# Performance work log

Measured on AMD Instinct MI355X. Metric: run time of the kernel, lower is better.

## Reference

```python
import jax, jax.numpy as jnp
import numpy as np

B, E, CIN, O = 2, 50000, 8, 128


def _mesh_conv(x, gemm, w, b):
    # MeshCNN MeshConv: x (B,C,E), gemm (B,E,4) neighbor indices, w (O,C,5), b (O,)
    # gather 4 GeMM neighbors per edge, build 5 symmetric features, 1x5 conv
    neigh = jax.vmap(lambda xb, gb: xb[:, gb])(x, gemm)  # (B,C,E,4)
    f1, f2, f3, f4 = neigh[..., 0], neigh[..., 1], neigh[..., 2], neigh[..., 3]
    G = jnp.stack([x, f1 + f3, f2 + f4, jnp.abs(f1 - f3), jnp.abs(f2 - f4)], axis=-1)  # (B,C,E,5)
    return jnp.einsum('bces,ocs->boe', G, w) + b[None, :, None]


def _inorm(x, eps=1e-5):
    # InstanceNorm (no affine, biased variance) over the edge dim, per (batch, channel)
    m = jnp.mean(x, axis=-1, keepdims=True)
    v = jnp.var(x, axis=-1, keepdims=True)
    return (x - m) * jax.lax.rsqrt(v + eps)


def _conv1(x, w, b):
    # 1x1 Conv1d: x (B,C,E), w (O,C)
    return jnp.einsum('bce,oc->boe', x, w) + b[None, :, None]


def setup_inputs() -> dict:
    key = jax.random.key(0)
    ks = jax.random.split(key, 16)

    def W(k, shape, fan):
        return jax.random.normal(k, shape, jnp.float32) * np.float32(1.0 / np.sqrt(fan))

    d = {}
    d['fe'] = jax.random.normal(ks[0], (B, CIN, E), jnp.float32)
    d['gemm'] = jax.random.randint(ks[1], (B, E, 4), 0, E)
    # first-stage MeshConvs: geometry branch (5 ch) and position branch (3 ch)
    d['w_e1'] = W(ks[2], (O, 5, 5), 25);       d['b_e1'] = jnp.zeros((O,), jnp.float32)
    d['w_p1'] = W(ks[3], (O, 3, 5), 15);       d['b_p1'] = jnp.zeros((O,), jnp.float32)
    # residual-block MeshConvs (blocks=1)
    d['w_e2'] = W(ks[4], (O, O, 5), O * 5);    d['b_e2'] = jnp.zeros((O,), jnp.float32)
    d['w_p2'] = W(ks[5], (O, O, 5), O * 5);    d['b_p2'] = jnp.zeros((O,), jnp.float32)
    # Attn(in_dim=O)
    d['wa'] = W(ks[6], (O // 4, O), O);        d['ba'] = jnp.zeros((O // 4,), jnp.float32)
    d['wb'] = W(ks[7], (O // 4, O), O);        d['bb'] = jnp.zeros((O // 4,), jnp.float32)
    d['wal'] = W(ks[8], (O // 2, O // 2), O // 2);  d['bal'] = jnp.zeros((O // 2,), jnp.float32)
    d['wbl'] = W(ks[9], (O // 2, O // 2), O // 2);  d['bbl'] = jnp.zeros((O // 2,), jnp.float32)
    d['wat'] = W(ks[10], (O // 2, O // 2, 5), O // 2 * 5); d['bat'] = jnp.zeros((O // 2,), jnp.float32)
    d['wbt'] = W(ks[11], (O // 2, O // 2, 5), O // 2 * 5); d['bbt'] = jnp.zeros((O // 2,), jnp.float32)
    d['waf'] = W(ks[12], (O, O), O);           d['baf'] = jnp.zeros((O,), jnp.float32)
    d['wbf'] = W(ks[13], (O, O), O);           d['bbf'] = jnp.zeros((O,), jnp.float32)
    return d


def reference(fe, gemm, w_e1, b_e1, w_p1, b_p1, w_e2, b_e2, w_p2, b_p2,
              wa, ba, wb, bb, wal, bal, wbl, bbl, wat, bat, wbt, bbt,
              waf, baf, wbf, bbf):
    # DownConv (8-channel input path): split into edge (5) and point (3) branches
    fe_e, fe_p = fe[:, :5, :], fe[:, 5:, :]
    x1_e = jax.nn.relu(_inorm(_mesh_conv(fe_e, gemm, w_e1, b_e1)))
    x2_e = jax.nn.relu(_inorm(_mesh_conv(x1_e, gemm, w_e2, b_e2)) + x1_e)
    x1_p = jax.nn.relu(_inorm(_mesh_conv(fe_p, gemm, w_p1, b_p1)))
    x2_p = jax.nn.relu(_inorm(_mesh_conv(x1_p, gemm, w_p2, b_p2)) + x1_p)
    # Attn fusion
    x_all = jnp.concatenate([_conv1(x2_e, wa, ba), _conv1(x2_p, wb, bb)], axis=1)  # (B, O/2, E)
    x_a_two = jnp.concatenate([_conv1(x_all, wal, bal), _mesh_conv(x_all, gemm, wat, bat)], axis=1)
    x_b_two = jnp.concatenate([_conv1(x_all, wbl, bbl), _mesh_conv(x_all, gemm, wbt, bbt)], axis=1)
    wA = jax.nn.sigmoid(_inorm(_conv1(x_a_two, waf, baf)))  # (B,O,E)
    wB = jax.nn.sigmoid(_inorm(_conv1(x_b_two, wbf, bbf)))
    weights = jax.nn.softmax(jnp.stack([wA, wB], axis=1), axis=1)  # (B,2,O,E)
    agg = x2_e * weights[:, 0] + x2_p * weights[:, 1]
    # x2_ep = cat(x2_e, x2_p); also emit the attention-fused combine (before_pool)
    return jnp.concatenate([x2_e, x2_p, agg], axis=1)  # (B, 3*O, E)
```

## Files before the change

kernel.cpp:

```cpp
#include <hip/hip_runtime.h>
#include <cstdio>
#include <math.h>


#define E_TOT 50000
#define B_TOT 2
#define TILE_E 64
#define NBLK ((E_TOT + TILE_E - 1) / TILE_E)

typedef _Float16 half_t;
typedef __attribute__((ext_vector_type(4))) _Float16 h4;
typedef __attribute__((ext_vector_type(8))) _Float16 h8;
typedef __attribute__((ext_vector_type(4))) float f32x4;

__device__ __forceinline__ float sigmoidf_(float x) {
    return 1.0f / (1.0f + __expf(-x));
}
__device__ __forceinline__ h8 habs8(h8 x) {
    union { h8 h; unsigned int u[4]; } v;
    v.h = x;
#pragma unroll
    for (int i = 0; i < 4; ++i) v.u[i] &= 0x7FFF7FFFu;
    return v.h;
}

#define OFF_W1E   0
#define OFF_W1P   8192
#define OFF_WTE2  16384
#define OFF_WTP2  98304
#define OFF_WHA   180224
#define OFF_WHB   221184
#define OFF_WTA   262144
#define OFF_WTB   266240
#define OFF_WTAF  270336
#define OFF_WTBF  286720
#define WARENA_N  303104

__global__ __launch_bounds__(256)
void wprep_k(half_t* __restrict__ wa_,
             const float* __restrict__ w_e1, const float* __restrict__ w_p1,
             const float* __restrict__ w_e2, const float* __restrict__ w_p2,
             const float* __restrict__ wat,  const float* __restrict__ wbt,
             const float* __restrict__ wa,   const float* __restrict__ wb,
             const float* __restrict__ wal,  const float* __restrict__ wbl,
             const float* __restrict__ waf,  const float* __restrict__ wbf)
{
    int idx = blockIdx.x * 256 + threadIdx.x;
    switch (blockIdx.y) {
    case 0: if (idx < 8192) { int o = idx >> 6, k = idx & 63, s = k >> 3, cc = k & 7;
            float v = (s < 5 && cc < 5) ? w_e1[o * 25 + cc * 5 + s] : 0.f;
            wa_[OFF_W1E + idx] = (half_t)v; } break;
    case 1: if (idx < 8192) { int o = idx >> 6, k = idx & 63, s = k >> 3, cc = k & 7;
            float v = (s < 5 && cc >= 5) ? w_p1[o * 15 + (cc - 5) * 5 + s] : 0.f;
            wa_[OFF_W1P + idx] = (half_t)v; } break;
    case 2: if (idx < 81920) { int o = idx / 640, r = idx % 640, s = r >> 7, c = r & 127;
            wa_[OFF_WTE2 + idx] = (half_t)w_e2[(o * 128 + c) * 5 + s]; } break;
    case 3: if (idx < 81920) { int o = idx / 640, r = idx % 640, s = r >> 7, c = r & 127;
            wa_[OFF_WTP2 + idx] = (half_t)w_p2[(o * 128 + c) * 5 + s]; } break;
    case 4: if (idx < 40960) { int o = idx / 320, r = idx % 320, s = r >> 6, c = r & 63;
            float v = (o < 64) ? (s == 0 ? wal[o * 64 + c] : 0.f)
                               : wat[((o - 64) * 64 + c) * 5 + s];
            wa_[OFF_WHA + idx] = (half_t)v; } break;
    case 5: if (idx < 40960) { int o = idx / 320, r = idx % 320, s = r >> 6, c = r & 63;
            float v = (o < 64) ? (s == 0 ? wbl[o * 64 + c] : 0.f)
                               : wbt[((o - 64) * 64 + c) * 5 + s];
            wa_[OFF_WHB + idx] = (half_t)v; } break;
    case 6: if (idx < 4096)  wa_[OFF_WTA  + idx] = (half_t)wa[idx];  break;
    case 7: if (idx < 4096)  wa_[OFF_WTB  + idx] = (half_t)wb[idx];  break;
    case 8: if (idx < 16384) wa_[OFF_WTAF + idx] = (half_t)waf[idx]; break;
    case 9: if (idx < 16384) wa_[OFF_WTBF + idx] = (half_t)wbf[idx]; break;
    }
}

__global__ __launch_bounds__(256)
void transpose_in_k(const float* __restrict__ fe, float* __restrict__ fet)
{
    int b = blockIdx.z;
    int e = blockIdx.x * 256 + threadIdx.x;
    if (e >= E_TOT) return;
    float v[8];
#pragma unroll
    for (int c = 0; c < 8; ++c)
        v[c] = fe[((long)b * 8 + c) * E_TOT + e];
    float4* dst = (float4*)&fet[((long)b * E_TOT + e) * 8];
    dst[0] = make_float4(v[0], v[1], v[2], v[3]);
    dst[1] = make_float4(v[4], v[5], v[6], v[7]);
}

__global__ __launch_bounds__(512)
void mesh1_both_k(const float* __restrict__ fet, const int* __restrict__ gemm,
                  const half_t* __restrict__ war,
                  const float* __restrict__ be1, const float* __restrict__ bp1,
                  half_t* __restrict__ tmpe, half_t* __restrict__ tmpp,
                  float* __restrict__ parte, float* __restrict__ partp)
{
    __shared__ h8 Gl[64 * 8];
    __shared__ int nidx[64][4];

    const int tid  = threadIdx.x;
    const int b    = blockIdx.y;
    const int e0   = blockIdx.x * TILE_E;
    const int lane = tid & 63;
    const int wv   = tid >> 6;
    const int l15  = lane & 15;
    const int kg   = lane >> 4;
    const int br   = wv >> 2;
    const int o0   = (wv & 3) * 32;

    const float* xb = fet + (long)b * E_TOT * 8;

    if (tid < 256) {
        int e = tid >> 2, s = tid & 3;
        int eg = e0 + e;
        nidx[e][s] = (eg < E_TOT) ? gemm[((long)b * E_TOT + eg) * 4 + s] : 0;
    }
    __syncthreads();

    {
        int e = tid >> 3, g = tid & 7;
        int eg = e0 + e;
        int se = (eg < E_TOT) ? eg : 0;
        h8 r;
        if (g == 0) {
            const float* p = xb + (long)se * 8;
            float4 v0 = *(const float4*)p, v1 = *(const float4*)(p + 4);
            r[0] = (half_t)v0.x; r[1] = (half_t)v0.y; r[2] = (half_t)v0.z; r[3] = (half_t)v0.w;
            r[4] = (half_t)v1.x; r[5] = (half_t)v1.y; r[6] = (half_t)v1.z; r[7] = (half_t)v1.w;
        } else if (g <= 4) {
            int ia = (g == 1 || g == 3) ? 0 : 1;
            const float* pa = xb + (long)nidx[e][ia] * 8;
            const float* pb = xb + (long)nidx[e][ia + 2] * 8;
            float4 a0 = *(const float4*)pa, a1 = *(const float4*)(pa + 4);
            float4 b0 = *(const float4*)pb, b1 = *(const float4*)(pb + 4);
            float aa[8] = {a0.x, a0.y, a0.z, a0.w, a1.x, a1.y, a1.z, a1.w};
            float bb[8] = {b0.x, b0.y, b0.z, b0.w, b1.x, b1.y, b1.z, b1.w};
            if (g <= 2) {
#pragma unroll
                for (int j = 0; j < 8; ++j) r[j] = (half_t)(aa[j] + bb[j]);
            } else {
#pragma unroll
                for (int j = 0; j < 8; ++j) r[j] = (half_t)fabsf(aa[j] - bb[j]);
            }
        } else {
#pragma unroll
            for (int j = 0; j < 8; ++j) r[j] = (half_t)0.f;
        }
        Gl[(e * 8 + g) ^ (e & 7)] = r;
    }
    __syncthreads();

    f32x4 acc[4][2];
#pragma unroll
    for (int mt = 0; mt < 4; ++mt)
#pragma unroll
        for (int nt = 0; nt < 2; ++nt)
#pragma unroll
            for (int j = 0; j < 4; ++j) acc[mt][nt][j] = 0.f;

    const half_t* wt = war + (br ? OFF_W1P : OFF_W1E);
#pragma unroll
    for (int ks = 0; ks < 2; ++ks) {
        h8 bw[2];
#pragma unroll
        for (int nt = 0; nt < 2; ++nt)
            bw[nt] = *(const h8*)(wt + (long)(o0 + nt * 16 + l15) * 64 + ks * 32 + kg * 8);
#pragma unroll
        for (int mt = 0; mt < 4; ++mt) {
            int row = mt * 16 + l15;
            h8 a = Gl[row * 8 + ((ks * 4 + kg) ^ (row & 7))];
#pragma unroll
            for (int nt = 0; nt < 2; ++nt)
                acc[mt][nt] = __builtin_amdgcn_mfma_f32_16x16x32_f16(a, bw[nt], acc[mt][nt], 0, 0, 0);
        }
    }

    const float* bias = br ? bp1 : be1;
    half_t* yb = (br ? tmpp : tmpe) + (long)b * E_TOT * 128;
    float* part = br ? partp : parte;
    float bv[2], s1[2], s2[2];
#pragma unroll
    for (int nt = 0; nt < 2; ++nt) {
        bv[nt] = bias[o0 + nt * 16 + l15];
        s1[nt] = 0.f; s2[nt] = 0.f;
    }
#pragma unroll
    for (int mt = 0; mt < 4; ++mt) {
        int ebase = e0 + mt * 16 + (kg << 2);
#pragma unroll
        for (int j = 0; j < 4; ++j) {
            if (ebase + j < E_TOT) {
#pragma unroll
                for (int nt = 0; nt < 2; ++nt) {
                    float v = acc[mt][nt][j] + bv[nt];
                    yb[(long)(ebase + j) * 128 + o0 + nt * 16 + l15] = (half_t)v;
                    s1[nt] += v; s2[nt] += v * v;
                }
            }
        }
    }
#pragma unroll
    for (int nt = 0; nt < 2; ++nt) {
        s1[nt] += __shfl_xor(s1[nt], 16); s1[nt] += __shfl_xor(s1[nt], 32);
        s2[nt] += __shfl_xor(s2[nt], 16); s2[nt] += __shfl_xor(s2[nt], 32);
    }
    if (lane < 16) {
        long pb = ((long)b * NBLK + blockIdx.x) * 128;
#pragma unroll
        for (int nt = 0; nt < 2; ++nt) {
            part[(pb + o0 + nt * 16 + lane) * 2 + 0] = s1[nt];
            part[(pb + o0 + nt * 16 + lane) * 2 + 1] = s2[nt];
        }
    }
}

__global__ __launch_bounds__(512)
void mesh2p_k(const half_t* __restrict__ x1e, const half_t* __restrict__ x1p,
              const int* __restrict__ gemm, const half_t* __restrict__ war,
              const float* __restrict__ be, const float* __restrict__ bp,
              half_t* __restrict__ tmpe, half_t* __restrict__ tmpp,
              float* __restrict__ parte, float* __restrict__ partp)
{
    __shared__ h8 A[1024];
    __shared__ h8 Bs[1024];
    __shared__ int nidx[64][4];

    const int tid  = threadIdx.x;
    const int br   = blockIdx.y;
    const int b    = blockIdx.z;
    const int e0   = blockIdx.x * TILE_E;
    const int lane = tid & 63;
    const int wv   = tid >> 6;
    const int l15  = lane & 15;
    const int kg   = lane >> 4;
    const int o0   = wv * 16;

    const half_t* xb = (br ? x1p : x1e) + (long)b * E_TOT * 128;
    const half_t* wt = war + (br ? OFF_WTP2 : OFF_WTE2);

    if (tid < 256) {
        int e = tid >> 2, s = tid & 3;
        int eg = e0 + e;
        nidx[e][s] = (eg < E_TOT) ? gemm[((long)b * E_TOT + eg) * 4 + s] : 0;
    }
    __syncthreads();

    int te[2], tc[2], ts[2];
#pragma unroll
    for (int t = 0; t < 2; ++t) {
        int q = t * 512 + tid;
        te[t] = q >> 4; tc[t] = q & 15;
        ts[t] = (te[t] * 16 + tc[t]) ^ (te[t] & 7);
    }

#pragma unroll
    for (int t = 0; t < 2; ++t) {
        int eg = e0 + te[t];
        int se = (eg < E_TOT) ? eg : 0;
        A[ts[t]] = *(const h8*)(xb + (long)se * 128 + tc[t] * 8);
    }
    h8 rA[2], rB[2];
#pragma unroll
    for (int t = 0; t < 2; ++t) {
        rA[t] = *(const h8*)(xb + (long)nidx[te[t]][0] * 128 + tc[t] * 8);
        rB[t] = *(const h8*)(xb + (long)nidx[te[t]][2] * 128 + tc[t] * 8);
    }
    __syncthreads();

    f32x4 acc[4];
#pragma unroll
    for (int mt = 0; mt < 4; ++mt)
#pragma unroll
        for (int j = 0; j < 4; ++j) acc[mt][j] = 0.f;

    auto chunk = [&](const h8* buf, int s) {
#pragma unroll
        for (int ks = 0; ks < 4; ++ks) {
            h8 bw = *(const h8*)(wt + ((long)(o0 + l15) * 5 + s) * 128 + ks * 32 + kg * 8);
#pragma unroll
            for (int mt = 0; mt < 4; ++mt) {
                int row = mt * 16 + l15;
                h8 a = buf[row * 16 + ((ks * 4 + kg) ^ (row & 7))];
                acc[mt] = __builtin_amdgcn_mfma_f32_16x16x32_f16(a, bw, acc[mt], 0, 0, 0);
            }
        }
    };

    chunk(A, 0);
    __syncthreads();

#pragma unroll
    for (int t = 0; t < 2; ++t) {
        Bs[ts[t]] = rA[t] + rB[t];
        A[ts[t]]  = habs8(rA[t] - rB[t]);
    }
#pragma unroll
    for (int t = 0; t < 2; ++t) {
        rA[t] = *(const h8*)(xb + (long)nidx[te[t]][1] * 128 + tc[t] * 8);
        rB[t] = *(const h8*)(xb + (long)nidx[te[t]][3] * 128 + tc[t] * 8);
    }
    __syncthreads();

    chunk(Bs, 1);
    chunk(A, 3);
    __syncthreads();

#pragma unroll
    for (int t = 0; t < 2; ++t) {
        Bs[ts[t]] = rA[t] + rB[t];
        A[ts[t]]  = habs8(rA[t] - rB[t]);
    }
    __syncthreads();

    chunk(Bs, 2);
    chunk(A, 4);

    const float* bias = br ? bp : be;
    half_t* yb = (br ? tmpp : tmpe) + (long)b * E_TOT * 128;
    float* part = br ? partp : parte;
    float bv = bias[o0 + l15];
    float s1 = 0.f, s2 = 0.f;
#pragma unroll
    for (int mt = 0; mt < 4; ++mt) {
        int ebase = e0 + mt * 16 + (kg << 2);
#pragma unroll
        for (int j = 0; j < 4; ++j) {
            if (ebase + j < E_TOT) {
                float v = acc[mt][j] + bv;
                yb[(long)(ebase + j) * 128 + o0 + l15] = (half_t)v;
                s1 += v; s2 += v * v;
            }
        }
    }
    s1 += __shfl_xor(s1, 16); s1 += __shfl_xor(s1, 32);
    s2 += __shfl_xor(s2, 16); s2 += __shfl_xor(s2, 32);
    if (lane < 16) {
        long pb = ((long)b * NBLK + blockIdx.x) * 128;
        part[(pb + o0 + lane) * 2 + 0] = s1;
        part[(pb + o0 + lane) * 2 + 1] = s2;
    }
}

__global__ __launch_bounds__(512)
void heads2_k(const half_t* __restrict__ xall, const int* __restrict__ gemm,
              const half_t* __restrict__ war,
              const float* __restrict__ bal, const float* __restrict__ bbl,
              const float* __restrict__ bat, const float* __restrict__ bbt,
              half_t* __restrict__ xa2, half_t* __restrict__ xb2)
{
    __shared__ h8 C0[512], C1[512], C2[512];
    __shared__ int nidx[64][4];

    const int tid  = threadIdx.x;
    const int b    = blockIdx.y;
    const int e0   = blockIdx.x * TILE_E;
    const int lane = tid & 63;
    const int wv   = tid >> 6;
    const int hd   = wv >> 2;
    const int o0   = (wv & 3) * 32;
    const int l15  = lane & 15;
    const int kg   = lane >> 4;

    const half_t* xb = xall + (long)b * E_TOT * 64;

    if (tid < 256) {
        int e = tid >> 2, s = tid & 3;
        int eg = e0 + e;
        nidx[e][s] = (eg < E_TOT) ? gemm[((long)b * E_TOT + eg) * 4 + s] : 0;
    }
    __syncthreads();

    const int te = tid >> 3, tc = tid & 7;
    const int tslot = (te * 8 + tc) ^ (te & 7);

    {
        int eg = e0 + te;
        int se = (eg < E_TOT) ? eg : 0;
        C0[tslot] = *(const h8*)(xb + (long)se * 64 + tc * 8);
    }
    h8 rA, rB;
    {
        int na = nidx[te][0], nb = nidx[te][2];
        rA = *(const h8*)(xb + (long)na * 64 + tc * 8);
        rB = *(const h8*)(xb + (long)nb * 64 + tc * 8);
    }
    __syncthreads();

    f32x4 acc[4][2];
#pragma unroll
    for (int mt = 0; mt < 4; ++mt)
#pragma unroll
        for (int nt = 0; nt < 2; ++nt)
#pragma unroll
            for (int j = 0; j < 4; ++j) acc[mt][nt][j] = 0.f;

    const half_t* wt = war + (hd ? OFF_WHB : OFF_WHA);
    auto chunk = [&](const h8* buf, int s) {
#pragma unroll
        for (int ks = 0; ks < 2; ++ks) {
            h8 bw0 = *(const h8*)(wt + ((long)(o0 + l15) * 5 + s) * 64 + ks * 32 + kg * 8);
            h8 bw1 = *(const h8*)(wt + ((long)(o0 + 16 + l15) * 5 + s) * 64 + ks * 32 + kg * 8);
#pragma unroll
            for (int mt = 0; mt < 4; ++mt) {
                int row = mt * 16 + l15;
                h8 a = buf[row * 8 + ((ks * 4 + kg) ^ (row & 7))];
                acc[mt][0] = __builtin_amdgcn_mfma_f32_16x16x32_f16(a, bw0, acc[mt][0], 0, 0, 0);
                acc[mt][1] = __builtin_amdgcn_mfma_f32_16x16x32_f16(a, bw1, acc[mt][1], 0, 0, 0);
            }
        }
    };

    chunk(C0, 0);
    __syncthreads();
    {
        C1[tslot] = rA + rB;
        C2[tslot] = habs8(rA - rB);
        int na = nidx[te][1], nb = nidx[te][3];
        rA = *(const h8*)(xb + (long)na * 64 + tc * 8);
        rB = *(const h8*)(xb + (long)nb * 64 + tc * 8);
    }
    __syncthreads();
    chunk(C1, 1);
    chunk(C2, 3);
    __syncthreads();
    {
        C1[tslot] = rA + rB;
        C2[tslot] = habs8(rA - rB);
    }
    __syncthreads();
    chunk(C1, 2);
    chunk(C2, 4);

    half_t* yb = (hd ? xb2 : xa2) + (long)b * E_TOT * 128;
    float bv[2];
#pragma unroll
    for (int nt = 0; nt < 2; ++nt) {
        int o = o0 + nt * 16 + l15;
        bv[nt] = (o < 64) ? (hd ? bbl[o] : bal[o]) : (hd ? bbt[o - 64] : bat[o - 64]);
    }
#pragma unroll
    for (int mt = 0; mt < 4; ++mt) {
        int ebase = e0 + mt * 16 + (kg << 2);
#pragma unroll
        for (int j = 0; j < 4; ++j) {
            if (ebase + j < E_TOT) {
#pragma unroll
                for (int nt = 0; nt < 2; ++nt)
                    yb[(long)(ebase + j) * 128 + o0 + nt * 16 + l15] =
                        (half_t)(acc[mt][nt][j] + bv[nt]);
            }
        }
    }
}

__global__ __launch_bounds__(512)
void gates_k(const half_t* __restrict__ xa2, const half_t* __restrict__ xb2,
             const half_t* __restrict__ war,
             const float* __restrict__ baf, const float* __restrict__ bbf,
             half_t* __restrict__ tmpe, half_t* __restrict__ tmpp,
             float* __restrict__ parte, float* __restrict__ partp)
{
    __shared__ h8 Gl[64 * 16];

    const int tid  = threadIdx.x;
    const int br   = blockIdx.y;
    const int b    = blockIdx.z;
    const int e0   = blockIdx.x * TILE_E;
    const int lane = tid & 63;
    const int wv   = tid >> 6;
    const int l15  = lane & 15;
    const int kg   = lane >> 4;
    const int o0   = wv * 16;

    const half_t* xb = (br ? xb2 : xa2) + (long)b * E_TOT * 128;
    const half_t* wt = war + (br ? OFF_WTBF : OFF_WTAF);

#pragma unroll
    for (int t = 0; t < 2; ++t) {
        int q = t * 512 + tid;
        int e = q >> 4, c8 = q & 15;
        int eg = e0 + e;
        int se = (eg < E_TOT) ? eg : 0;
        Gl[(e * 16 + c8) ^ (e & 7)] = *(const h8*)(xb + (long)se * 128 + c8 * 8);
    }
    __syncthreads();

    f32x4 acc[4];
#pragma unroll
    for (int mt = 0; mt < 4; ++mt)
#pragma unroll
        for (int j = 0; j < 4; ++j) acc[mt][j] = 0.f;

#pragma unroll
    for (int ks = 0; ks < 4; ++ks) {
        h8 bw = *(const h8*)(wt + (long)(o0 + l15) * 128 + ks * 32 + kg * 8);
#pragma unroll
        for (int mt = 0; mt < 4; ++mt) {
            int row = mt * 16 + l15;
            h8 a = Gl[row * 16 + ((ks * 4 + kg) ^ (row & 7))];
            acc[mt] = __builtin_amdgcn_mfma_f32_16x16x32_f16(a, bw, acc[mt], 0, 0, 0);
        }
    }

    const float* bias = br ? bbf : baf;
    half_t* yb = (br ? tmpp : tmpe) + (long)b * E_TOT * 128;
    float* part = br ? partp : parte;
    float bv = bias[o0 + l15];
    float s1 = 0.f, s2 = 0.f;
#pragma unroll
    for (int mt = 0; mt < 4; ++mt) {
        int ebase = e0 + mt * 16 + (kg << 2);
#pragma unroll
        for (int j = 0; j < 4; ++j) {
            if (ebase + j < E_TOT) {
                float v = acc[mt][j] + bv;
                yb[(long)(ebase + j) * 128 + o0 + l15] = (half_t)v;
                s1 += v; s2 += v * v;
            }
        }
    }
    s1 += __shfl_xor(s1, 16); s1 += __shfl_xor(s1, 32);
    s2 += __shfl_xor(s2, 16); s2 += __shfl_xor(s2, 32);
    if (lane < 16) {
        long pb = ((long)b * NBLK + blockIdx.x) * 128;
        part[(pb + o0 + lane) * 2 + 0] = s1;
        part[(pb + o0 + lane) * 2 + 1] = s2;
    }
}

__global__ __launch_bounds__(256)
void xall_k(const half_t* __restrict__ x2e, const half_t* __restrict__ x2p,
            const half_t* __restrict__ war,
            const float* __restrict__ ba, const float* __restrict__ bb,
            half_t* __restrict__ xall)
{
    __shared__ h8 Gl[64 * 16];

    const int tid  = threadIdx.x;
    const int br   = blockIdx.y;
    const int b    = blockIdx.z;
    const int e0   = blockIdx.x * TILE_E;
    const int lane = tid & 63;
    const int wv   = tid >> 6;
    const int l15  = lane & 15;
    const int kg   = lane >> 4;
    const int eoff = wv * 16;

    const half_t* xb = (br ? x2p : x2e) + (long)b * E_TOT * 128;
    const half_t* wt = war + (br ? OFF_WTB : OFF_WTA);

#pragma unroll
    for (int t = 0; t < 4; ++t) {
        int q = t * 256 + tid;
        int e = q >> 4, c8 = q & 15;
        int eg = e0 + e;
        int se = (eg < E_TOT) ? eg : 0;
        Gl[(e * 16 + c8) ^ (e & 7)] = *(const h8*)(xb + (long)se * 128 + c8 * 8);
    }
    __syncthreads();

    f32x4 acc[2];
#pragma unroll
    for (int nt = 0; nt < 2; ++nt)
#pragma unroll
        for (int j = 0; j < 4; ++j) acc[nt][j] = 0.f;

#pragma unroll
    for (int ks = 0; ks < 4; ++ks) {
        h8 bw[2];
#pragma unroll
        for (int nt = 0; nt < 2; ++nt)
            bw[nt] = *(const h8*)(wt + (long)(nt * 16 + l15) * 128 + ks * 32 + kg * 8);
        int row = eoff + l15;
        h8 a = Gl[row * 16 + ((ks * 4 + kg) ^ (row & 7))];
#pragma unroll
        for (int nt = 0; nt < 2; ++nt)
            acc[nt] = __builtin_amdgcn_mfma_f32_16x16x32_f16(a, bw[nt], acc[nt], 0, 0, 0);
    }

    const float* bias = br ? bb : ba;
    half_t* yb = xall + (long)b * E_TOT * 64;
    int oOff = br * 32;
#pragma unroll
    for (int nt = 0; nt < 2; ++nt) {
        float bv = bias[nt * 16 + l15];
        int ebase = e0 + eoff + (kg << 2);
#pragma unroll
        for (int j = 0; j < 4; ++j) {
            if (ebase + j < E_TOT)
                yb[(long)(ebase + j) * 64 + oOff + nt * 16 + l15] = (half_t)(acc[nt][j] + bv);
        }
    }
}

__global__ __launch_bounds__(256)
void stats2_k(const float* __restrict__ parte, const float* __restrict__ partp,
              float* __restrict__ statse, float* __restrict__ statsp)
{
    int g = blockIdx.x;
    int br = g >> 8, rem = g & 255, b = rem >> 7, o = rem & 127;
    const float* part = br ? partp : parte;
    float* stats = br ? statsp : statse;
    int tid = threadIdx.x;
    float s1 = 0.f, s2 = 0.f;
    for (int k = tid; k < NBLK; k += 256) {
        long base = (((long)b * NBLK + k) * 128 + o) * 2;
        s1 += part[base];
        s2 += part[base + 1];
    }
#pragma unroll
    for (int d = 1; d < 64; d <<= 1) {
        s1 += __shfl_xor(s1, d);
        s2 += __shfl_xor(s2, d);
    }
    __shared__ float r1[4], r2[4];
    int wv = tid >> 6;
    if ((tid & 63) == 0) { r1[wv] = s1; r2[wv] = s2; }
    __syncthreads();
    if (tid == 0) {
        s1 = r1[0] + r1[1] + r1[2] + r1[3];
        s2 = r2[0] + r2[1] + r2[2] + r2[3];
        float mean = s1 / (float)E_TOT;
        float var  = s2 / (float)E_TOT - mean * mean;
        var = fmaxf(var, 0.f);
        stats[(b * 128 + o) * 2 + 0] = mean;
        stats[(b * 128 + o) * 2 + 1] = rsqrtf(var + 1e-5f);
    }
}

__global__ __launch_bounds__(256)
void norm_act2_k(const half_t* __restrict__ tmpe, const half_t* __restrict__ tmpp,
                 const float* __restrict__ statse, const float* __restrict__ statsp,
                 half_t* __restrict__ x1e, half_t* __restrict__ x1p)
{
    const long PER = (long)B_TOT * E_TOT * 16;
    long q = (long)blockIdx.x * 256 + threadIdx.x;
    if (q >= 2 * PER) return;
    int br = (q >= PER);
    q -= (long)br * PER;
    const half_t* src = br ? tmpp : tmpe;
    const float* stats = br ? statsp : statse;
    half_t* dst = br ? x1p : x1e;
    long idx = q * 8;
    int c = (int)(idx & 127);
    int b = (int)((idx >> 7) / E_TOT);
    h8 v = *(const h8*)&src[idx];
    h8 r;
#pragma unroll
    for (int j = 0; j < 8; ++j) {
        float2 st = *(const float2*)&stats[(b * 128 + c + j) * 2];
        float t = ((float)v[j] - st.x) * st.y;
        r[j] = (half_t)fmaxf(t, 0.f);
    }
    *(h8*)&dst[idx] = r;
}

__global__ __launch_bounds__(256)
void normres2_k(const half_t* __restrict__ tmpe, const half_t* __restrict__ tmpp,
                const half_t* __restrict__ x1e, const half_t* __restrict__ x1p,
                const float* __restrict__ statse, const float* __restrict__ statsp,
                float* __restrict__ outb,
                half_t* __restrict__ x2e, half_t* __restrict__ x2p)
{
    __shared__ float T[32 * 68];
    int br = blockIdx.y >> 2, cg = blockIdx.y & 3;
    int b = blockIdx.z;
    int e0 = blockIdx.x * 64;
    int tid = threadIdx.x;
    const half_t* xin = br ? tmpp : tmpe;
    const half_t* res = br ? x1p : x1e;
    const float* stats = br ? statsp : statse;
    half_t* x2b = br ? x2p : x2e;
    int sect = br * 128;
#pragma unroll
    for (int i = 0; i < 2; ++i) {
        int q = tid + i * 256;
        int e = q >> 3, cq = q & 7;
        int eg = e0 + e;
        int se = (eg < E_TOT) ? eg : (E_TOT - 1);
        int c = cg * 32 + cq * 4;
        long base = ((long)b * E_TOT + se) * 128 + c;
        h4 v4 = *(const h4*)&xin[base];
        h4 r4 = *(const h4*)&res[base];
        h4 o4;
#pragma unroll
        for (int j = 0; j < 4; ++j) {
            float2 st = *(const float2*)&stats[(b * 128 + c + j) * 2];
            float t = ((float)v4[j] - st.x) * st.y + (float)r4[j];
            t = fmaxf(t, 0.f);
            T[(cq * 4 + j) * 68 + e] = t;
            o4[j] = (half_t)t;
        }
        if (eg < E_TOT) *(h4*)&x2b[base] = o4;
    }
    __syncthreads();
#pragma unroll
    for (int i = 0; i < 2; ++i) {
        int q = tid + i * 256;
        int cl = q >> 4, eq = q & 15;
        int e4 = e0 + eq * 4;
        int cglob = sect + cg * 32 + cl;
        float4 v = *(const float4*)&T[cl * 68 + eq * 4];
        long obase = ((long)b * 384 + cglob) * E_TOT + e4;
        if (e4 + 3 < E_TOT) {
            *(float4*)&outb[obase] = v;
        } else {
            const float* vp = &v.x;
            for (int j = 0; j < 4; ++j)
                if (e4 + j < E_TOT) outb[obase + j] = vp[j];
        }
    }
}

__global__ __launch_bounds__(256)
void gate_agg2_k(const half_t* __restrict__ tA, const half_t* __restrict__ tB,
                 const float* __restrict__ statsA, const float* __restrict__ statsB,
                 const half_t* __restrict__ x2e, const half_t* __restrict__ x2p,
                 float* __restrict__ outb)
{
    __shared__ float T[32 * 68];
    int b = blockIdx.z, cg = blockIdx.y;
    int e0 = blockIdx.x * 64;
    int tid = threadIdx.x;
#pragma unroll
    for (int i = 0; i < 2; ++i) {
        int q = tid + i * 256;
        int e = q >> 3, cq = q & 7;
        int eg = e0 + e;
        int se = (eg < E_TOT) ? eg : (E_TOT - 1);
        int c = cg * 32 + cq * 4;
        long base = ((long)b * E_TOT + se) * 128 + c;
        h4 a4 = *(const h4*)&tA[base];
        h4 b4 = *(const h4*)&tB[base];
        h4 xe4 = *(const h4*)&x2e[base];
        h4 xp4 = *(const h4*)&x2p[base];
#pragma unroll
        for (int j = 0; j < 4; ++j) {
            float2 sa = *(const float2*)&statsA[(b * 128 + c + j) * 2];
            float2 sb = *(const float2*)&statsB[(b * 128 + c + j) * 2];
            float na = sigmoidf_(((float)a4[j] - sa.x) * sa.y);
            float nb = sigmoidf_(((float)b4[j] - sb.x) * sb.y);
            float s = sigmoidf_(na - nb);
            T[(cq * 4 + j) * 68 + e] = (float)xe4[j] * s + (float)xp4[j] * (1.f - s);
        }
    }
    __syncthreads();
#pragma unroll
    for (int i = 0; i < 2; ++i) {
        int q = tid + i * 256;
        int cl = q >> 4, eq = q & 15;
        int e4 = e0 + eq * 4;
        int cglob = cg * 32 + cl;
        float4 v = *(const float4*)&T[cl * 68 + eq * 4];
        long ab = ((long)b * 384 + 256 + cglob) * E_TOT + e4;
        if (e4 + 3 < E_TOT) {
            *(float4*)&outb[ab] = v;
        } else {
            const float* vp = &v.x;
            for (int j = 0; j < 4; ++j)
                if (e4 + j < E_TOT) outb[ab + j] = vp[j];
        }
    }
}

extern "C" void kernel_launch(void* const* d_in, const int* in_sizes, int n_in,
                              void* d_out, int out_size, void* d_ws, size_t ws_size,
                              hipStream_t stream)
{
    const float* fe   = (const float*)d_in[0];
    const int*   gemm = (const int*)  d_in[1];
    const float* w_e1 = (const float*)d_in[2];  const float* b_e1 = (const float*)d_in[3];
    const float* w_p1 = (const float*)d_in[4];  const float* b_p1 = (const float*)d_in[5];
    const float* w_e2 = (const float*)d_in[6];  const float* b_e2 = (const float*)d_in[7];
    const float* w_p2 = (const float*)d_in[8];  const float* b_p2 = (const float*)d_in[9];
    const float* wa   = (const float*)d_in[10]; const float* ba   = (const float*)d_in[11];
    const float* wb   = (const float*)d_in[12]; const float* bb   = (const float*)d_in[13];
    const float* wal  = (const float*)d_in[14]; const float* bal  = (const float*)d_in[15];
    const float* wbl  = (const float*)d_in[16]; const float* bbl  = (const float*)d_in[17];
    const float* wat  = (const float*)d_in[18]; const float* bat  = (const float*)d_in[19];
    const float* wbt  = (const float*)d_in[20]; const float* bbt  = (const float*)d_in[21];
    const float* waf  = (const float*)d_in[22]; const float* baf  = (const float*)d_in[23];
    const float* wbf  = (const float*)d_in[24]; const float* bbf  = (const float*)d_in[25];
    float* out = (float*)d_out;

    const long EB = (long)E_TOT;

    char* wp = (char*)d_ws;
    auto alloc = [&](size_t bytes) -> void* {
        void* r = (void*)wp;
        wp += (bytes + 255) & ~(size_t)255;
        return r;
    };
    float*  FET    = (float*)alloc((size_t)B_TOT * EB * 8 * 4);
    half_t* TMP_E  = (half_t*)alloc((size_t)B_TOT * EB * 128 * 2);
    half_t* TMP_P  = (half_t*)alloc((size_t)B_TOT * EB * 128 * 2);
    half_t* X1E    = (half_t*)alloc((size_t)B_TOT * EB * 128 * 2);
    half_t* X1P    = (half_t*)alloc((size_t)B_TOT * EB * 128 * 2);
    half_t* X2E    = (half_t*)alloc((size_t)B_TOT * EB * 128 * 2);
    half_t* X2P    = (half_t*)alloc((size_t)B_TOT * EB * 128 * 2);
    half_t* XALL   = (half_t*)alloc((size_t)B_TOT * EB * 64 * 2);
    float*  PART_E = (float*)alloc((size_t)B_TOT * NBLK * 128 * 2 * 4);
    float*  PART_P = (float*)alloc((size_t)B_TOT * NBLK * 128 * 2 * 4);
    float*  STATSE = (float*)alloc((size_t)B_TOT * 128 * 2 * 4);
    float*  STATSP = (float*)alloc((size_t)B_TOT * 128 * 2 * 4);
    half_t* WAR    = (half_t*)alloc((size_t)WARENA_N * 2);

    if ((size_t)(wp - (char*)d_ws) > ws_size) {
        fprintf(stderr, "kernel_launch: ws too small (%zu < %zu)\n",
                ws_size, (size_t)(wp - (char*)d_ws));
        return;
    }

    half_t* XA2 = X1E;
    half_t* XB2 = X1P;

    dim3 blk256(256), blk512(512);
    dim3 gI(NBLK, B_TOT);
    dim3 gE2(NBLK, 2, B_TOT);
    dim3 gT((E_TOT + 255) / 256, 1, B_TOT);
    dim3 gN8(NBLK, 8, B_TOT);
    dim3 gN4(NBLK, 4, B_TOT);
    int gA2 = (int)((2 * (long)B_TOT * EB * 16 + 255) / 256);

    wprep_k<<<dim3(320, 10, 1), blk256, 0, stream>>>(WAR,
        w_e1, w_p1, w_e2, w_p2, wat, wbt, wa, wb, wal, wbl, waf, wbf);
    transpose_in_k<<<gT, blk256, 0, stream>>>(fe, FET);

    mesh1_both_k<<<gI, blk512, 0, stream>>>(FET, gemm, WAR, b_e1, b_p1,
        TMP_E, TMP_P, PART_E, PART_P);
    stats2_k<<<512, blk256, 0, stream>>>(PART_E, PART_P, STATSE, STATSP);
    norm_act2_k<<<gA2, blk256, 0, stream>>>(TMP_E, TMP_P, STATSE, STATSP, X1E, X1P);

    mesh2p_k<<<gE2, blk512, 0, stream>>>(X1E, X1P, gemm, WAR, b_e2, b_p2,
        TMP_E, TMP_P, PART_E, PART_P);
    stats2_k<<<512, blk256, 0, stream>>>(PART_E, PART_P, STATSE, STATSP);
    normres2_k<<<gN8, blk256, 0, stream>>>(TMP_E, TMP_P, X1E, X1P, STATSE, STATSP,
        out, X2E, X2P);

    xall_k<<<gE2, blk256, 0, stream>>>(X2E, X2P, WAR, ba, bb, XALL);

    heads2_k<<<gI, blk512, 0, stream>>>(XALL, gemm, WAR, bal, bbl, bat, bbt, XA2, XB2);

    gates_k<<<gE2, blk512, 0, stream>>>(XA2, XB2, WAR, baf, bbf,
        TMP_E, TMP_P, PART_E, PART_P);
    stats2_k<<<512, blk256, 0, stream>>>(PART_E, PART_P, STATSE, STATSP);
    gate_agg2_k<<<gN4, blk256, 0, stream>>>(TMP_E, TMP_P, STATSE, STATSP,
        X2E, X2P, out);
}
```

Measured before the change: 370.4 us.

## Fuse attention heads and gate 1x1 conv into one kernel via LDS staging

The heads kernel now keeps its 128-channel per-edge outputs in shared memory and immediately runs the gate 1x1 conv MFMA on them, writing gate pre-activations and instance-norm partial sums. This removes the separate gates kernel and the global write and read of the XA2/XB2 intermediates. The mesh2 kernel is also restructured so neighbor loads are no longer prefetched into registers ahead of compute, with stage and compute done in sequence. That change reduces register pressure but loses some load/compute overlap.

```diff
diff --git a/kernel.cpp b/kernel.cpp
--- a/kernel.cpp
+++ b/kernel.cpp
@@ -214,14 +214,14 @@
 }
 
 __global__ __launch_bounds__(512)
-void mesh2p_k(const half_t* __restrict__ x1e, const half_t* __restrict__ x1p,
-              const int* __restrict__ gemm, const half_t* __restrict__ war,
-              const float* __restrict__ be, const float* __restrict__ bp,
-              half_t* __restrict__ tmpe, half_t* __restrict__ tmpp,
-              float* __restrict__ parte, float* __restrict__ partp)
-{
-    __shared__ h8 A[1024];
-    __shared__ h8 Bs[1024];
+void mesh2_k(const half_t* __restrict__ x1e, const half_t* __restrict__ x1p,
+             const int* __restrict__ gemm, const half_t* __restrict__ war,
+             const float* __restrict__ be, const float* __restrict__ bp,
+             half_t* __restrict__ tmpe, half_t* __restrict__ tmpp,
+             float* __restrict__ parte, float* __restrict__ partp)
+{
+    __shared__ h8 GlA[64 * 16];
+    __shared__ h8 GlB[64 * 16];
     __shared__ int nidx[64][4];
 
     const int tid  = threadIdx.x;
@@ -242,29 +242,30 @@
         int eg = e0 + e;
         nidx[e][s] = (eg < E_TOT) ? gemm[((long)b * E_TOT + eg) * 4 + s] : 0;
     }
-    __syncthreads();
-
-    int te[2], tc[2], ts[2];
-#pragma unroll
-    for (int t = 0; t < 2; ++t) {
-        int q = t * 512 + tid;
-        te[t] = q >> 4; tc[t] = q & 15;
-        ts[t] = (te[t] * 16 + tc[t]) ^ (te[t] & 7);
-    }
-
-#pragma unroll
-    for (int t = 0; t < 2; ++t) {
-        int eg = e0 + te[t];
-        int se = (eg < E_TOT) ? eg : 0;
-        A[ts[t]] = *(const h8*)(xb + (long)se * 128 + tc[t] * 8);
-    }
-    h8 rA[2], rB[2];
-#pragma unroll
-    for (int t = 0; t < 2; ++t) {
-        rA[t] = *(const h8*)(xb + (long)nidx[te[t]][0] * 128 + tc[t] * 8);
-        rB[t] = *(const h8*)(xb + (long)nidx[te[t]][2] * 128 + tc[t] * 8);
-    }
-    __syncthreads();
+
+    auto stage_self = [&](h8* dst) {
+#pragma unroll
+        for (int t = 0; t < 2; ++t) {
+            int q = t * 512 + tid;
+            int e = q >> 4, c8 = q & 15;
+            int eg = e0 + e;
+            int se = (eg < E_TOT) ? eg : 0;
+            dst[(e * 16 + c8) ^ (e & 7)] = *(const h8*)(xb + (long)se * 128 + c8 * 8);
+        }
+    };
+    auto stage_pair = [&](h8* dstS, h8* dstD, int ia, int ib) {
+#pragma unroll
+        for (int t = 0; t < 2; ++t) {
+            int q = t * 512 + tid;
+            int e = q >> 4, c8 = q & 15;
+            int na = nidx[e][ia], nb = nidx[e][ib];
+            h8 a  = *(const h8*)(xb + (long)na * 128 + c8 * 8);
+            h8 bq = *(const h8*)(xb + (long)nb * 128 + c8 * 8);
+            int slot = (e * 16 + c8) ^ (e & 7);
+            dstS[slot] = a + bq;
+            dstD[slot] = habs8(a - bq);
+        }
+    };
 
     f32x4 acc[4];
 #pragma unroll
@@ -272,7 +273,7 @@
 #pragma unroll
         for (int j = 0; j < 4; ++j) acc[mt][j] = 0.f;
 
-    auto chunk = [&](const h8* buf, int s) {
+    auto compute_chunk = [&](const h8* buf, int s) {
 #pragma unroll
         for (int ks = 0; ks < 4; ++ks) {
             h8 bw = *(const h8*)(wt + ((long)(o0 + l15) * 5 + s) * 128 + ks * 32 + kg * 8);
@@ -285,34 +286,19 @@
         }
     };
 
-    chunk(A, 0);
-    __syncthreads();
-
-#pragma unroll
-    for (int t = 0; t < 2; ++t) {
-        Bs[ts[t]] = rA[t] + rB[t];
-        A[ts[t]]  = habs8(rA[t] - rB[t]);
-    }
-#pragma unroll
-    for (int t = 0; t < 2; ++t) {
-        rA[t] = *(const h8*)(xb + (long)nidx[te[t]][1] * 128 + tc[t] * 8);
-        rB[t] = *(const h8*)(xb + (long)nidx[te[t]][3] * 128 + tc[t] * 8);
-    }
-    __syncthreads();
-
-    chunk(Bs, 1);
-    chunk(A, 3);
-    __syncthreads();
-
-#pragma unroll
-    for (int t = 0; t < 2; ++t) {
-        Bs[ts[t]] = rA[t] + rB[t];
-        A[ts[t]]  = habs8(rA[t] - rB[t]);
-    }
-    __syncthreads();
-
-    chunk(Bs, 2);
-    chunk(A, 4);
+    stage_self(GlA);
+    __syncthreads();
+    compute_chunk(GlA, 0);
+    __syncthreads();
+    stage_pair(GlA, GlB, 0, 2);
+    __syncthreads();
+    compute_chunk(GlA, 1);
+    compute_chunk(GlB, 3);
+    __syncthreads();
+    stage_pair(GlA, GlB, 1, 3);
+    __syncthreads();
+    compute_chunk(GlA, 2);
+    compute_chunk(GlB, 4);
 
     const float* bias = br ? bp : be;
     half_t* yb = (br ? tmpp : tmpe) + (long)b * E_TOT * 128;
@@ -341,13 +327,15 @@
 }
 
 __global__ __launch_bounds__(512)
-void heads2_k(const half_t* __restrict__ xall, const int* __restrict__ gemm,
-              const half_t* __restrict__ war,
-              const float* __restrict__ bal, const float* __restrict__ bbl,
-              const float* __restrict__ bat, const float* __restrict__ bbt,
-              half_t* __restrict__ xa2, half_t* __restrict__ xb2)
-{
-    __shared__ h8 C0[512], C1[512], C2[512];
+void heads_gates_k(const half_t* __restrict__ xall, const int* __restrict__ gemm,
+                   const half_t* __restrict__ war,
+                   const float* __restrict__ bal, const float* __restrict__ bbl,
+                   const float* __restrict__ bat, const float* __restrict__ bbt,
+                   const float* __restrict__ baf, const float* __restrict__ bbf,
+                   half_t* __restrict__ tmpe, half_t* __restrict__ tmpp,
+                   float* __restrict__ parte, float* __restrict__ partp)
+{
+    __shared__ h8 arena[2048];
     __shared__ int nidx[64][4];
 
     const int tid  = threadIdx.x;
@@ -360,6 +348,10 @@
     const int l15  = lane & 15;
     const int kg   = lane >> 4;
 
+    h8* C0 = arena;
+    h8* C1 = arena + 512;
+    h8* C2 = arena + 1024;
+
     const half_t* xb = xall + (long)b * E_TOT * 64;
 
     if (tid < 256) {
@@ -379,9 +371,8 @@
     }
     h8 rA, rB;
     {
-        int na = nidx[te][0], nb = nidx[te][2];
-        rA = *(const h8*)(xb + (long)na * 64 + tc * 8);
-        rB = *(const h8*)(xb + (long)nb * 64 + tc * 8);
+        rA = *(const h8*)(xb + (long)nidx[te][0] * 64 + tc * 8);
+        rB = *(const h8*)(xb + (long)nidx[te][2] * 64 + tc * 8);
     }
     __syncthreads();
 
@@ -414,9 +405,8 @@
     {
         C1[tslot] = rA + rB;
         C2[tslot] = habs8(rA - rB);
-        int na = nidx[te][1], nb = nidx[te][3];
-        rA = *(const h8*)(xb + (long)na * 64 + tc * 8);
-        rB = *(const h8*)(xb + (long)nb * 64 + tc * 8);
+        rA = *(const h8*)(xb + (long)nidx[te][1] * 64 + tc * 8);
+        rB = *(const h8*)(xb + (long)nidx[te][3] * 64 + tc * 8);
     }
     __syncthreads();
     chunk(C1, 1);
@@ -429,14 +419,60 @@
     __syncthreads();
     chunk(C1, 2);
     chunk(C2, 4);
-
-    half_t* yb = (hd ? xb2 : xa2) + (long)b * E_TOT * 128;
-    float bv[2];
-#pragma unroll
-    for (int nt = 0; nt < 2; ++nt) {
-        int o = o0 + nt * 16 + l15;
-        bv[nt] = (o < 64) ? (hd ? bbl[o] : bal[o]) : (hd ? bbt[o - 64] : bat[o - 64]);
-    }
+    __syncthreads();
+
+    {
+        half_t* X = (half_t*)(arena + hd * 1024);
+        float bv[2];
+#pragma unroll
+        for (int nt = 0; nt < 2; ++nt) {
+            int o = o0 + nt * 16 + l15;
+            bv[nt] = (o < 64) ? (hd ? bbl[o] : bal[o]) : (hd ? bbt[o - 64] : bat[o - 64]);
+        }
+#pragma unroll
+        for (int mt = 0; mt < 4; ++mt) {
+#pragma unroll
+            for (int j = 0; j < 4; ++j) {
+                int e = mt * 16 + (kg << 2) + j;
+#pragma unroll
+                for (int nt = 0; nt < 2; ++nt) {
+                    int c = o0 + nt * 16 + l15;
+                    int slot = (e * 16 + (c >> 3)) ^ (e & 7);
+                    X[slot * 8 + (c & 7)] = (half_t)(acc[mt][nt][j] + bv[nt]);
+                }
+            }
+        }
+    }
+    __syncthreads();
+
+    f32x4 g[4][2];
+#pragma unroll
+    for (int mt = 0; mt < 4; ++mt)
+#pragma unroll
+        for (int nt = 0; nt < 2; ++nt)
+#pragma unroll
+            for (int j = 0; j < 4; ++j) g[mt][nt][j] = 0.f;
+
+    const half_t* wtg = war + (hd ? OFF_WTBF : OFF_WTAF);
+    const h8* X = arena + hd * 1024;
+#pragma unroll
+    for (int ks = 0; ks < 4; ++ks) {
+        h8 bw0 = *(const h8*)(wtg + (long)(o0 + l15) * 128 + ks * 32 + kg * 8);
+        h8 bw1 = *(const h8*)(wtg + (long)(o0 + 16 + l15) * 128 + ks * 32 + kg * 8);
+#pragma unroll
+        for (int mt = 0; mt < 4; ++mt) {
+            int row = mt * 16 + l15;
+            h8 a = X[row * 16 + ((ks * 4 + kg) ^ (row & 7))];
+            g[mt][0] = __builtin_amdgcn_mfma_f32_16x16x32_f16(a, bw0, g[mt][0], 0, 0, 0);
+            g[mt][1] = __builtin_amdgcn_mfma_f32_16x16x32_f16(a, bw1, g[mt][1], 0, 0, 0);
+        }
+    }
+
+    const float* biasg = hd ? bbf : baf;
+    half_t* yb = (hd ? tmpp : tmpe) + (long)b * E_TOT * 128;
+    float* part = hd ? partp : parte;
+    float bg[2] = {biasg[o0 + l15], biasg[o0 + 16 + l15]};
+    float s1[2] = {0.f, 0.f}, s2[2] = {0.f, 0.f};
 #pragma unroll
     for (int mt = 0; mt < 4; ++mt) {
         int ebase = e0 + mt * 16 + (kg << 2);
@@ -444,86 +480,26 @@
         for (int j = 0; j < 4; ++j) {
             if (ebase + j < E_TOT) {
 #pragma unroll
-                for (int nt = 0; nt < 2; ++nt)
-                    yb[(long)(ebase + j) * 128 + o0 + nt * 16 + l15] =
-                        (half_t)(acc[mt][nt][j] + bv[nt]);
+                for (int nt = 0; nt < 2; ++nt) {
+                    float v = g[mt][nt][j] + bg[nt];
+                    yb[(long)(ebase + j) * 128 + o0 + nt * 16 + l15] = (half_t)v;
+                    s1[nt] += v; s2[nt] += v * v;
+                }
             }
         }
     }
-}
-
-__global__ __launch_bounds__(512)
-void gates_k(const half_t* __restrict__ xa2, const half_t* __restrict__ xb2,
-             const half_t* __restrict__ war,
-             const float* __restrict__ baf, const float* __restrict__ bbf,
-             half_t* __restrict__ tmpe, half_t* __restrict__ tmpp,
-             float* __restrict__ parte, float* __restrict__ partp)
-{
-    __shared__ h8 Gl[64 * 16];
-
-    const int tid  = threadIdx.x;
-    const int br   = blockIdx.y;
-    const int b    = blockIdx.z;
-    const int e0   = blockIdx.x * TILE_E;
-    const int lane = tid & 63;
-    const int wv   = tid >> 6;
-    const int l15  = lane & 15;
-    const int kg   = lane >> 4;
-    const int o0   = wv * 16;
-
-    const half_t* xb = (br ? xb2 : xa2) + (long)b * E_TOT * 128;
-    const half_t* wt = war + (br ? OFF_WTBF : OFF_WTAF);
-
-#pragma unroll
-    for (int t = 0; t < 2; ++t) {
-        int q = t * 512 + tid;
-        int e = q >> 4, c8 = q & 15;
-        int eg = e0 + e;
-        int se = (eg < E_TOT) ? eg : 0;
-        Gl[(e * 16 + c8) ^ (e & 7)] = *(const h8*)(xb + (long)se * 128 + c8 * 8);
-    }
-    __syncthreads();
-
-    f32x4 acc[4];
-#pragma unroll
-    for (int mt = 0; mt < 4; ++mt)
-#pragma unroll
-        for (int j = 0; j < 4; ++j) acc[mt][j] = 0.f;
-
-#pragma unroll
-    for (int ks = 0; ks < 4; ++ks) {
-        h8 bw = *(const h8*)(wt + (long)(o0 + l15) * 128 + ks * 32 + kg * 8);
-#pragma unroll
-        for (int mt = 0; mt < 4; ++mt) {
-            int row = mt * 16 + l15;
-            h8 a = Gl[row * 16 + ((ks * 4 + kg) ^ (row & 7))];
-            acc[mt] = __builtin_amdgcn_mfma_f32_16x16x32_f16(a, bw, acc[mt], 0, 0, 0);
-        }
-    }
-
-    const float* bias = br ? bbf : baf;
-    half_t* yb = (br ? tmpp : tmpe) + (long)b * E_TOT * 128;
-    float* part = br ? partp : parte;
-    float bv = bias[o0 + l15];
-    float s1 = 0.f, s2 = 0.f;
-#pragma unroll
-    for (int mt = 0; mt < 4; ++mt) {
-        int ebase = e0 + mt * 16 + (kg << 2);
-#pragma unroll
-        for (int j = 0; j < 4; ++j) {
-            if (ebase + j < E_TOT) {
-                float v = acc[mt][j] + bv;
-                yb[(long)(ebase + j) * 128 + o0 + l15] = (half_t)v;
-                s1 += v; s2 += v * v;
-            }
-        }
-    }
-    s1 += __shfl_xor(s1, 16); s1 += __shfl_xor(s1, 32);
-    s2 += __shfl_xor(s2, 16); s2 += __shfl_xor(s2, 32);
+#pragma unroll
+    for (int nt = 0; nt < 2; ++nt) {
+        s1[nt] += __shfl_xor(s1[nt], 16); s1[nt] += __shfl_xor(s1[nt], 32);
+        s2[nt] += __shfl_xor(s2[nt], 16); s2[nt] += __shfl_xor(s2[nt], 32);
+    }
     if (lane < 16) {
         long pb = ((long)b * NBLK + blockIdx.x) * 128;
-        part[(pb + o0 + lane) * 2 + 0] = s1;
-        part[(pb + o0 + lane) * 2 + 1] = s2;
+#pragma unroll
+        for (int nt = 0; nt < 2; ++nt) {
+            part[(pb + o0 + nt * 16 + lane) * 2 + 0] = s1[nt];
+            part[(pb + o0 + nt * 16 + lane) * 2 + 1] = s2[nt];
+        }
     }
 }
 
@@ -810,9 +786,6 @@
         return;
     }
 
-    half_t* XA2 = X1E;
-    half_t* XB2 = X1P;
-
     dim3 blk256(256), blk512(512);
     dim3 gI(NBLK, B_TOT);
     dim3 gE2(NBLK, 2, B_TOT);
@@ -830,7 +803,7 @@
     stats2_k<<<512, blk256, 0, stream>>>(PART_E, PART_P, STATSE, STATSP);
     norm_act2_k<<<gA2, blk256, 0, stream>>>(TMP_E, TMP_P, STATSE, STATSP, X1E, X1P);
 
-    mesh2p_k<<<gE2, blk512, 0, stream>>>(X1E, X1P, gemm, WAR, b_e2, b_p2,
+    mesh2_k<<<gE2, blk512, 0, stream>>>(X1E, X1P, gemm, WAR, b_e2, b_p2,
         TMP_E, TMP_P, PART_E, PART_P);
     stats2_k<<<512, blk256, 0, stream>>>(PART_E, PART_P, STATSE, STATSP);
     normres2_k<<<gN8, blk256, 0, stream>>>(TMP_E, TMP_P, X1E, X1P, STATSE, STATSP,
@@ -838,10 +811,9 @@
 
     xall_k<<<gE2, blk256, 0, stream>>>(X2E, X2P, WAR, ba, bb, XALL);
 
-    heads2_k<<<gI, blk512, 0, stream>>>(XALL, gemm, WAR, bal, bbl, bat, bbt, XA2, XB2);
-
-    gates_k<<<gE2, blk512, 0, stream>>>(XA2, XB2, WAR, baf, bbf,
-        TMP_E, TMP_P, PART_E, PART_P);
+    heads_gates_k<<<gI, blk512, 0, stream>>>(XALL, gemm, WAR,
+        bal, bbl, bat, bbt, baf, bbf, TMP_E, TMP_P, PART_E, PART_P);
+
     stats2_k<<<512, blk256, 0, stream>>>(PART_E, PART_P, STATSE, STATSP);
     gate_agg2_k<<<gN4, blk256, 0, stream>>>(TMP_E, TMP_P, STATSE, STATSP,
         X2E, X2P, out);
```

Measured after the change: 345.9 us. 6.6% less time.
